# Optimization experiments

Measured on AMD Instinct MI355X. Metric: run time of the kernel, lower is better.

Reference implementation:

```python
import jax, jax.numpy as jnp
import numpy as np

B = 16384
D = 384
K = 256
BETAS = (0.05, 0.25, 0.6)  # per-level commitment costs


def setup_inputs() -> dict:
    key = jax.random.key(0)
    k0, k1, k2, kc0, kc1, kc2 = jax.random.split(key, 6)
    return {
        "l0": jax.random.normal(k0, (B, 4, D), dtype=jnp.float32),
        "l1": jax.random.normal(k1, (B, 16, D), dtype=jnp.float32),
        "l2": jax.random.normal(k2, (B, 16, D), dtype=jnp.float32),
        "cb0": jax.random.normal(kc0, (K, D), dtype=jnp.float32),
        "cb1": jax.random.normal(kc1, (K, D), dtype=jnp.float32),
        "cb2": jax.random.normal(kc2, (K, D), dtype=jnp.float32),
    }


def _vq(x, cb, beta):
    # x: (B, T, D), cb: (K, D) -> d2: (B, T, K)
    d2 = (jnp.sum(x * x, axis=-1, keepdims=True)
          - 2.0 * jnp.einsum('btd,kd->btk', x, cb)
          + jnp.sum(cb * cb, axis=-1))
    idx = jnp.argmin(d2, axis=-1)            # (B, T) nearest codebook entry
    q = cb[idx]                              # (B, T, D) gather
    # EMA-VQ: codebook updated by EMA, loss is commitment term only
    loss = beta * jnp.mean((jax.lax.stop_gradient(q) - x) ** 2)
    q_st = x + jax.lax.stop_gradient(q - x)  # straight-through estimator
    return q_st, loss, idx


def reference(l0, l1, l2, cb0, cb1, cb2):
    q0, loss0, idx0 = _vq(l0, cb0, BETAS[0])
    q1, loss1, idx1 = _vq(l1, cb1, BETAS[1])
    q2, loss2, idx2 = _vq(l2, cb2, BETAS[2])
    total_vq_loss = loss0 + loss1 + loss2
    return (q0, q1, q2, total_vq_loss, idx0, idx1, idx2)
```

## Files before the change

kernel.cpp:

```cpp
#include <hip/hip_runtime.h>

static constexpr int KN  = 256;
static constexpr int DD  = 384;
static constexpr int DD4 = 96;
static constexpr int TM  = 64;
#define FLAG_MARGIN 0.005f

typedef __attribute__((ext_vector_type(8)))  short bf16x8;
typedef __attribute__((ext_vector_type(16))) float f32x16;
typedef __attribute__((ext_vector_type(4)))  short short4v;

__device__ __forceinline__ unsigned short f2bf_rne(float x) {
  unsigned u = __float_as_uint(x);
  return (unsigned short)((u + 0x7fffu + ((u >> 16) & 1u)) >> 16);
}

__device__ __forceinline__ void g2lds16(const void* g, void* l) {
  __builtin_amdgcn_global_load_lds(
      (const __attribute__((address_space(1))) unsigned int*)g,
      (__attribute__((address_space(3))) unsigned int*)l, 16, 0, 0);
}

__device__ __forceinline__ float emu_sq_pairwise384(const float* __restrict__ p) {
  float S[4];
#pragma unroll
  for (int blk = 0; blk < 4; ++blk) {
    const float* b = p + blk * 96;
    float r[8];
#pragma unroll
    for (int l = 0; l < 8; ++l) r[l] = __fmul_rn(b[l], b[l]);
    for (int j = 8; j < 96; j += 8) {
#pragma unroll
      for (int l = 0; l < 8; ++l) r[l] = __fadd_rn(r[l], __fmul_rn(b[j + l], b[j + l]));
    }
    float t1 = __fadd_rn(__fadd_rn(r[0], r[1]), __fadd_rn(r[2], r[3]));
    float t2 = __fadd_rn(__fadd_rn(r[4], r[5]), __fadd_rn(r[6], r[7]));
    S[blk] = __fadd_rn(t1, t2);
  }
  return __fadd_rn(__fadd_rn(S[0], S[1]), __fadd_rn(S[2], S[3]));
}

__device__ __forceinline__ float emu_dot384_np(const float* __restrict__ x,
                                               const float* __restrict__ c) {
  float s[16];
#pragma unroll
  for (int t = 0; t < 16; ++t) s[t] = 0.f;
  for (int j = 0; j < 384; j += 16) {
#pragma unroll
    for (int t = 0; t < 16; ++t)
      s[t] = __fadd_rn(__fmul_rn(x[j + t], c[j + t]), s[t]);
  }
  float w0 = __fadd_rn(__fadd_rn(s[0], s[4]), __fadd_rn(s[8],  s[12]));
  float w1 = __fadd_rn(__fadd_rn(s[1], s[5]), __fadd_rn(s[9],  s[13]));
  float w2 = __fadd_rn(__fadd_rn(s[2], s[6]), __fadd_rn(s[10], s[14]));
  float w3 = __fadd_rn(__fadd_rn(s[3], s[7]), __fadd_rn(s[11], s[15]));
  return __fadd_rn(__fadd_rn(w0, w1), __fadd_rn(w2, w3));
}

__global__ __launch_bounds__(256) void prep_kernel(const float* __restrict__ c0,
                                                   const float* __restrict__ c1,
                                                   const float* __restrict__ c2,
                                                   float* __restrict__ e2,
                                                   double* __restrict__ delta,
                                                   short* __restrict__ fragbase) {
  int bid = blockIdx.x;
  if (bid < 3) {
    const float* cb = (bid == 0) ? c0 : ((bid == 1) ? c1 : c2);
    e2[bid * KN + threadIdx.x] = emu_sq_pairwise384(cb + (size_t)threadIdx.x * DD);
    if (threadIdx.x == 0) delta[bid] = 0.0;
    return;
  }
  int sb = bid - 3;
  int lvl = sb / 48;
  int blk48 = sb - lvl * 48;
  const float* cb = (lvl == 0) ? c0 : ((lvl == 1) ? c1 : c2);
  short* frag = fragbase + (size_t)lvl * 196608;
  int gid = blk48 * 256 + threadIdx.x;
  int e = gid / 48;
  int g = gid - e * 48;
  const float4* s4 = reinterpret_cast<const float4*>(cb) + (size_t)e * 96 + g * 2;
  float4 v0 = s4[0], v1 = s4[1];
  float xs[8] = {v0.x, v0.y, v0.z, v0.w, v1.x, v1.y, v1.z, v1.w};
  short h[8], l[8];
#pragma unroll
  for (int i = 0; i < 8; ++i) {
    h[i] = (short)f2bf_rne(xs[i]);
    float hf = __uint_as_float((unsigned)(unsigned short)h[i] << 16);
    l[i] = (short)f2bf_rne(xs[i] - hf);
  }
  int c = g >> 2, rem = g & 3, ks = rem >> 1, hs = rem & 1;
  int t = e >> 5, lane = (e & 31) + (hs << 5);
  size_t blk = (((size_t)(c * 8 + t) * 2 + ks) * 2);
  short* dh = frag + blk * 512 + lane * 8;
  short* dl = dh + 512;
  *reinterpret_cast<bf16x8*>(dh) = *reinterpret_cast<const bf16x8*>(h);
  *reinterpret_cast<bf16x8*>(dl) = *reinterpret_cast<const bf16x8*>(l);
}

__global__ __launch_bounds__(256) void vq_main(
    const float* __restrict__ X0, const float* __restrict__ X1, const float* __restrict__ X2,
    const float* __restrict__ C0, const float* __restrict__ C1, const float* __restrict__ C2,
    const short* __restrict__ FRAGBASE,
    const float* __restrict__ E2A,
    float* __restrict__ QBASE,
    float* __restrict__ IDXBASE,
    unsigned char* __restrict__ FLAGBASE,
    double* __restrict__ PART,
    int nb0, int nb1)
{
  __shared__ __align__(16) short cb_lds[16384];
  __shared__ __align__(16) short x_lds[4224];
  __shared__ int idx_s[TM];
  __shared__ float xx_s[TM];
  __shared__ float cand_b1[2][TM];
  __shared__ int   cand_i1[2][TM];
  __shared__ float cand_b2[2][TM];

  const int bid = blockIdx.x;
  int lvl, lb;
  if (bid < nb0)            { lvl = 0; lb = bid; }
  else if (bid < nb0 + nb1) { lvl = 1; lb = bid - nb0; }
  else                      { lvl = 2; lb = bid - nb0 - nb1; }
  const float* X  = (lvl == 0) ? X0 : ((lvl == 1) ? X1 : X2);
  const float* CBF32 = (lvl == 0) ? C0 : ((lvl == 1) ? C1 : C2);
  const short* CBFRAG = FRAGBASE + (size_t)lvl * 196608;
  const float* E2 = E2A + lvl * KN;
  const size_t rowbase = (lvl == 0) ? 0 : ((lvl == 1) ? (size_t)nb0 * TM
                                                      : (size_t)(nb0 + nb1) * TM);
  float* Q = QBASE + rowbase * DD;
  float* IDXO = IDXBASE + rowbase;
  unsigned char* FLAG = FLAGBASE + rowbase;
  const size_t row0 = (size_t)lb * TM;

  const float4* X4 = reinterpret_cast<const float4*>(X);

  f32x16 acc[4];
  {
    f32x16 z;
#pragma unroll
    for (int i = 0; i < 16; ++i) z[i] = 0.f;
#pragma unroll
    for (int ct = 0; ct < 4; ++ct) acc[ct] = z;
  }
  const int tid  = threadIdx.x;
  const int wid  = tid >> 6, lane = tid & 63;
  const int lr   = lane & 31, hi = lane >> 5;
  const int wr   = wid >> 1, wc = wid & 1;
  float xx0 = 0.f, xx1 = 0.f;

#pragma unroll 1
  for (int c = 0; c < 12; ++c) {
    {
      const char* gsrc = (const char*)CBFRAG + (size_t)c * 32768 + tid * 16;
#pragma unroll
      for (int s = 0; s < 8; ++s)
        g2lds16(gsrc + s * 4096, (char*)cb_lds + tid * 16 + s * 4096);
    }
#pragma unroll
    for (int i = 0; i < 2; ++i) {
      int idx = tid + i * 256;
      int r = idx >> 3, k4 = idx & 7;
      float4 v = X4[(row0 + (size_t)r) * DD4 + c * 8 + k4];
      float pp = v.x * v.x + v.y * v.y + v.z * v.z + v.w * v.w;
      if (i == 0) xx0 += pp; else xx1 += pp;
      float xs[4] = {v.x, v.y, v.z, v.w};
      short h[4], l[4];
#pragma unroll
      for (int e = 0; e < 4; ++e) {
        h[e] = (short)f2bf_rne(xs[e]);
        float hf = __uint_as_float((unsigned)(unsigned short)h[e] << 16);
        l[e] = (short)f2bf_rne(xs[e] - hf);
      }
      int rt = r >> 5, ks = k4 >> 2, hs = (k4 >> 1) & 1;
      int off_h = ((rt * 2 + ks) * 2) * 528 + hs * 264 + (r & 31) * 8 + (k4 & 1) * 4;
      *reinterpret_cast<short4v*>(&x_lds[off_h])       = *reinterpret_cast<short4v*>(h);
      *reinterpret_cast<short4v*>(&x_lds[off_h + 528]) = *reinterpret_cast<short4v*>(l);
    }
    __syncthreads();

#pragma unroll 1
    for (int ks = 0; ks < 2; ++ks) {
      const int abase = ((wr * 2 + ks) * 2) * 528 + hi * 264 + lr * 8;
      bf16x8 ah = *reinterpret_cast<const bf16x8*>(&x_lds[abase]);
      bf16x8 al = *reinterpret_cast<const bf16x8*>(&x_lds[abase + 528]);
      const bf16x8* bb = reinterpret_cast<const bf16x8*>(cb_lds);
#pragma unroll
      for (int ct = 0; ct < 4; ++ct) {
        int t = wc * 4 + ct;
        bf16x8 bh = bb[((t * 2 + ks) * 2 + 0) * 64 + lane];
        bf16x8 bl = bb[((t * 2 + ks) * 2 + 1) * 64 + lane];
        acc[ct] = __builtin_amdgcn_mfma_f32_32x32x16_bf16(ah, bh, acc[ct], 0, 0, 0);
        acc[ct] = __builtin_amdgcn_mfma_f32_32x32x16_bf16(ah, bl, acc[ct], 0, 0, 0);
        acc[ct] = __builtin_amdgcn_mfma_f32_32x32x16_bf16(al, bh, acc[ct], 0, 0, 0);
      }
    }
    __syncthreads();
  }

#pragma unroll
  for (int m = 1; m < 8; m <<= 1) {
    xx0 += __shfl_xor(xx0, m);
    xx1 += __shfl_xor(xx1, m);
  }
  if ((lane & 7) == 0) {
    xx_s[tid >> 3]        = xx0;
    xx_s[(tid >> 3) + 32] = xx1;
  }

  float e2v[4];
#pragma unroll
  for (int ct = 0; ct < 4; ++ct) e2v[ct] = E2[wc * 128 + ct * 32 + lr];

#pragma unroll
  for (int v = 0; v < 16; ++v) {
    int rloc = (v & 3) + 8 * (v >> 2) + 4 * hi;
    int row = wr * 32 + rloc;
    float b1 = 1e30f; int i1 = 0x7fffffff;
#pragma unroll
    for (int ct = 0; ct < 4; ++ct) {
      float sc = e2v[ct] - 2.0f * acc[ct][v];
      int col = wc * 128 + ct * 32 + lr;
      if (sc < b1) { b1 = sc; i1 = col; }
    }
#pragma unroll
    for (int m = 1; m < 32; m <<= 1) {
      float ob = __shfl_xor(b1, m);
      int   oi = __shfl_xor(i1, m);
      if (ob < b1 || (ob == b1 && oi < i1)) { b1 = ob; i1 = oi; }
    }
    float b2 = 1e30f;
#pragma unroll
    for (int ct = 0; ct < 4; ++ct) {
      float sc = e2v[ct] - 2.0f * acc[ct][v];
      int col = wc * 128 + ct * 32 + lr;
      if (col != i1 && sc < b2) b2 = sc;
    }
#pragma unroll
    for (int m = 1; m < 32; m <<= 1) {
      float ob = __shfl_xor(b2, m);
      if (ob < b2) b2 = ob;
    }
    if (lr == 0) {
      cand_b1[wc][row] = b1; cand_i1[wc][row] = i1; cand_b2[wc][row] = b2;
    }
  }
  __syncthreads();

  double lrow = 0.0;
  if (tid < TM) {
    float a1 = cand_b1[0][tid], a2 = cand_b2[0][tid];
    int   ai = cand_i1[0][tid];
    float c1 = cand_b1[1][tid], c2 = cand_b2[1][tid];
    int   ci = cand_i1[1][tid];
    float b1; int i1; float b2;
    if (c1 < a1 || (c1 == a1 && ci < ai)) {
      b1 = c1; i1 = ci; b2 = (a1 < c2) ? a1 : c2;
    } else {
      b1 = a1; i1 = ai; b2 = (c1 < a2) ? c1 : a2;
    }
    idx_s[tid] = i1;
    IDXO[row0 + tid] = (float)i1;
    FLAG[row0 + tid] = (b2 - b1 < FLAG_MARGIN) ? 1 : 0;
    lrow = (double)xx_s[tid] + (double)b1;
  }
  if (tid < 64) {
#pragma unroll
    for (int m = 1; m < 64; m <<= 1) lrow += __shfl_xor(lrow, m);
    if (tid == 0) PART[bid] = lrow;
  }
  __syncthreads();

  const float4* CB4 = reinterpret_cast<const float4*>(CBF32);
  float4* Q4 = reinterpret_cast<float4*>(Q);
  for (int i = tid; i < TM * DD4; i += 256) {
    int r = i / DD4;
    int cc = i - r * DD4;
    Q4[(row0 + (size_t)r) * DD4 + cc] = CB4[(size_t)idx_s[r] * DD4 + cc];
  }
}

__global__ __launch_bounds__(256) void vq_refine(
    const float* __restrict__ X0, const float* __restrict__ X1, const float* __restrict__ X2,
    const float* __restrict__ C0, const float* __restrict__ C1, const float* __restrict__ C2,
    const float* __restrict__ E2A,
    const unsigned char* __restrict__ F0, const unsigned char* __restrict__ F1,
    const unsigned char* __restrict__ F2,
    int r0, int r1, int r2,
    float* __restrict__ Q0, float* __restrict__ Q1, float* __restrict__ Q2,
    float* __restrict__ I0, float* __restrict__ I1, float* __restrict__ I2,
    double* __restrict__ DELTA)
{
  const int lane   = threadIdx.x & 63;
  const int gwave  = (blockIdx.x * blockDim.x + threadIdx.x) >> 6;
  const int nwaves = (gridDim.x * blockDim.x) >> 6;
  const int ntot = r0 + r1 + r2;

  for (int base = gwave * 64; base < ntot; base += nwaves * 64) {
    int lvl, lb;
    const float *X, *CB; const unsigned char* FLAG; float *Q, *IDXO;
    if (base < r0)           { lvl = 0; lb = base;            X = X0; CB = C0; FLAG = F0; Q = Q0; IDXO = I0; }
    else if (base < r0 + r1) { lvl = 1; lb = base - r0;       X = X1; CB = C1; FLAG = F1; Q = Q1; IDXO = I1; }
    else                     { lvl = 2; lb = base - r0 - r1;  X = X2; CB = C2; FLAG = F2; Q = Q2; IDXO = I2; }
    const float* E2EMU = E2A + lvl * KN;

    unsigned char f = FLAG[lb + lane];
    unsigned long long mask = __ballot(f != 0);
    while (mask) {
      int bit = __ffsll((long long)mask) - 1;
      mask &= mask - 1;
      const int r = lb + bit;
      const float* xr = X + (size_t)r * DD;
      const float xx = emu_sq_pairwise384(xr);

      float best = 1e30f; int bidx = 0x7fffffff;
#pragma unroll
      for (int t = 0; t < 4; ++t) {
        int k = lane * 4 + t;
        const float* ck = CB + (size_t)k * DD;
        float E = emu_dot384_np(xr, ck);
        float s = __fadd_rn(__fsub_rn(xx, __fmul_rn(2.0f, E)), E2EMU[k]);
        if (s < best || (s == best && k < bidx)) { best = s; bidx = k; }
      }
#pragma unroll
      for (int m = 1; m < 64; m <<= 1) {
        float ob = __shfl_xor(best, m);
        int   oi = __shfl_xor(bidx, m);
        if (ob < best || (ob == best && oi < bidx)) { best = ob; bidx = oi; }
      }

      const int old = (int)IDXO[r];
      if (bidx != old) {
        const float* cn = CB + (size_t)bidx * DD;
        const float* co = CB + (size_t)old * DD;
        double dl = 0.0;
        for (int d = lane; d < DD; d += 64) {
          float xv = xr[d];
          float qn = cn[d], qo = co[d];
          Q[(size_t)r * DD + d] = qn;
          double en = (double)qn - (double)xv;
          double eo = (double)qo - (double)xv;
          dl += en * en - eo * eo;
        }
#pragma unroll
        for (int m = 1; m < 64; m <<= 1) dl += __shfl_xor(dl, m);
        if (lane == 0) {
          atomicAdd(DELTA + lvl, dl);
          IDXO[r] = (float)bidx;
        }
      }
    }
  }
}

__global__ void finalize_kernel(const double* __restrict__ p0, int n0, double w0,
                                const double* __restrict__ p1, int n1, double w1,
                                const double* __restrict__ p2, int n2, double w2,
                                const double* __restrict__ delta,
                                float* __restrict__ out) {
  __shared__ double red[4];
  int tid = threadIdx.x;
  double s0 = 0.0, s1 = 0.0, s2 = 0.0;
  for (int i = tid; i < n0; i += 256) s0 += p0[i];
  for (int i = tid; i < n1; i += 256) s1 += p1[i];
  for (int i = tid; i < n2; i += 256) s2 += p2[i];
  double v = s0 * w0 + s1 * w1 + s2 * w2;
#pragma unroll
  for (int m = 1; m < 64; m <<= 1) v += __shfl_xor(v, m);
  if ((tid & 63) == 0) red[tid >> 6] = v;
  __syncthreads();
  if (tid == 0)
    out[0] = (float)(red[0] + red[1] + red[2] + red[3]
                     + delta[0] * w0 + delta[1] * w1 + delta[2] * w2);
}

extern "C" void kernel_launch(void* const* d_in, const int* in_sizes, int n_in,
                              void* d_out, int out_size, void* d_ws, size_t ws_size,
                              hipStream_t stream) {
  const float* l0  = (const float*)d_in[0];
  const float* l1  = (const float*)d_in[1];
  const float* l2  = (const float*)d_in[2];
  const float* cb0 = (const float*)d_in[3];
  const float* cb1 = (const float*)d_in[4];
  const float* cb2 = (const float*)d_in[5];

  const size_t n_q0 = (size_t)in_sizes[0];
  const size_t n_q1 = (size_t)in_sizes[1];
  const size_t n_q2 = (size_t)in_sizes[2];
  const int r0 = (int)(n_q0 / DD);
  const int r1 = (int)(n_q1 / DD);
  const int r2 = (int)(n_q2 / DD);

  float* out   = (float*)d_out;
  float* q0    = out;
  float* q1    = q0 + n_q0;
  float* q2    = q1 + n_q1;
  float* lossp = q2 + n_q2;
  float* idx0  = lossp + 1;
  float* idx1  = idx0 + r0;
  float* idx2  = idx1 + r1;

  float*  e2    = (float*)d_ws;
  double* part  = (double*)((char*)d_ws + 4096);
  double* delta = (double*)((char*)d_ws + 4096 + 73728);
  unsigned char* flag0 = (unsigned char*)d_ws + 4096 + 73728 + 1024;
  unsigned char* flag1 = flag0 + r0;
  unsigned char* flag2 = flag1 + r1;
  short* cbf0 = (short*)((char*)d_ws + (1 << 20));

  const int nb0 = r0 / TM, nb1 = r1 / TM, nb2 = r2 / TM;
  double* p0 = part;
  double* p1 = p0 + nb0;
  double* p2 = p1 + nb1;

  prep_kernel<<<147, 256, 0, stream>>>(cb0, cb1, cb2, e2, delta, cbf0);

  vq_main<<<nb0 + nb1 + nb2, 256, 0, stream>>>(
      l0, l1, l2, cb0, cb1, cb2, cbf0, e2,
      q0, idx0, flag0, part, nb0, nb1);

  vq_refine<<<512, 256, 0, stream>>>(l0, l1, l2, cb0, cb1, cb2, e2,
                                     flag0, flag1, flag2, r0, r1, r2,
                                     q0, q1, q2, idx0, idx1, idx2, delta);

  const double w0 = 0.05 / ((double)r0 * DD);
  const double w1 = 0.25 / ((double)r1 * DD);
  const double w2 = 0.60 / ((double)r2 * DD);
  finalize_kernel<<<1, 256, 0, stream>>>(p0, nb0, w0, p1, nb1, w1, p2, nb2, w2,
                                         delta, lossp);
}
```

Measured before the change: 770.7 us.

## Double-buffer codebook tiles and load X fragments straight into registers

Codebook chunks are now double-buffered in LDS and prefetched one chunk ahead, with a single barrier per iteration instead of two. The X rows are read from global memory directly into per-lane MFMA operand registers (register prefetch of the next chunk), which removes the x_lds staging buffer and its writes. The norm reduction becomes a single cross-half shuffle. In exchange each tile of X is loaded twice (once per column wave) and LDS use doubles for the codebook, which may reduce occupancy.

```diff
diff --git a/kernel.cpp b/kernel.cpp
--- a/kernel.cpp
+++ b/kernel.cpp
@@ -8,7 +8,6 @@
 
 typedef __attribute__((ext_vector_type(8)))  short bf16x8;
 typedef __attribute__((ext_vector_type(16))) float f32x16;
-typedef __attribute__((ext_vector_type(4)))  short short4v;
 
 __device__ __forceinline__ unsigned short f2bf_rne(float x) {
   unsigned u = __float_as_uint(x);
@@ -19,6 +18,19 @@
   __builtin_amdgcn_global_load_lds(
       (const __attribute__((address_space(1))) unsigned int*)g,
       (__attribute__((address_space(3))) unsigned int*)l, 16, 0, 0);
+}
+
+__device__ __forceinline__ void cvt8(float4 a, float4 b, bf16x8& h, bf16x8& l,
+                                     float& xx) {
+  float v[8] = {a.x, a.y, a.z, a.w, b.x, b.y, b.z, b.w};
+#pragma unroll
+  for (int i = 0; i < 8; ++i) {
+    xx += v[i] * v[i];
+    unsigned short hh = f2bf_rne(v[i]);
+    float hf = __uint_as_float((unsigned)hh << 16);
+    h[i] = (short)hh;
+    l[i] = (short)f2bf_rne(v[i] - hf);
+  }
 }
 
 __device__ __forceinline__ float emu_sq_pairwise384(const float* __restrict__ p) {
@@ -108,8 +120,7 @@
     double* __restrict__ PART,
     int nb0, int nb1)
 {
-  __shared__ __align__(16) short cb_lds[16384];
-  __shared__ __align__(16) short x_lds[4224];
+  __shared__ __align__(16) short cb_lds[2][16384];
   __shared__ int idx_s[TM];
   __shared__ float xx_s[TM];
   __shared__ float cand_b1[2][TM];
@@ -132,80 +143,69 @@
   unsigned char* FLAG = FLAGBASE + rowbase;
   const size_t row0 = (size_t)lb * TM;
 
-  const float4* X4 = reinterpret_cast<const float4*>(X);
-
-  f32x16 acc[4];
-  {
-    f32x16 z;
-#pragma unroll
-    for (int i = 0; i < 16; ++i) z[i] = 0.f;
-#pragma unroll
-    for (int ct = 0; ct < 4; ++ct) acc[ct] = z;
-  }
   const int tid  = threadIdx.x;
   const int wid  = tid >> 6, lane = tid & 63;
   const int lr   = lane & 31, hi = lane >> 5;
   const int wr   = wid >> 1, wc = wid & 1;
-  float xx0 = 0.f, xx1 = 0.f;
+
+  const float4* X4 = reinterpret_cast<const float4*>(X);
+  const float4* xrow = X4 + (row0 + (size_t)(wr * 32 + lr)) * DD4 + hi * 2;
+
+  f32x16 acc[4];
+  {
+    f32x16 z;
+#pragma unroll
+    for (int i = 0; i < 16; ++i) z[i] = 0.f;
+#pragma unroll
+    for (int ct = 0; ct < 4; ++ct) acc[ct] = z;
+  }
+  float xx = 0.f;
+
+  float4 xr0 = xrow[0], xr1 = xrow[1], xr2 = xrow[4], xr3 = xrow[5];
+  {
+    const char* gsrc = (const char*)CBFRAG + (size_t)tid * 16;
+#pragma unroll
+    for (int s = 0; s < 8; ++s)
+      g2lds16(gsrc + s * 4096, (char*)cb_lds[0] + tid * 16 + s * 4096);
+  }
+  __syncthreads();
 
 #pragma unroll 1
   for (int c = 0; c < 12; ++c) {
-    {
-      const char* gsrc = (const char*)CBFRAG + (size_t)c * 32768 + tid * 16;
+    bf16x8 ah0, al0, ah1, al1;
+    cvt8(xr0, xr1, ah0, al0, xx);
+    cvt8(xr2, xr3, ah1, al1, xx);
+
+    if (c < 11) {
+      const float4* xp = xrow + (c + 1) * 8;
+      xr0 = xp[0]; xr1 = xp[1]; xr2 = xp[4]; xr3 = xp[5];
+      const char* gsrc = (const char*)CBFRAG + (size_t)(c + 1) * 32768 + tid * 16;
+      char* dst = (char*)cb_lds[(c + 1) & 1] + tid * 16;
 #pragma unroll
       for (int s = 0; s < 8; ++s)
-        g2lds16(gsrc + s * 4096, (char*)cb_lds + tid * 16 + s * 4096);
-    }
-#pragma unroll
-    for (int i = 0; i < 2; ++i) {
-      int idx = tid + i * 256;
-      int r = idx >> 3, k4 = idx & 7;
-      float4 v = X4[(row0 + (size_t)r) * DD4 + c * 8 + k4];
-      float pp = v.x * v.x + v.y * v.y + v.z * v.z + v.w * v.w;
-      if (i == 0) xx0 += pp; else xx1 += pp;
-      float xs[4] = {v.x, v.y, v.z, v.w};
-      short h[4], l[4];
-#pragma unroll
-      for (int e = 0; e < 4; ++e) {
-        h[e] = (short)f2bf_rne(xs[e]);
-        float hf = __uint_as_float((unsigned)(unsigned short)h[e] << 16);
-        l[e] = (short)f2bf_rne(xs[e] - hf);
-      }
-      int rt = r >> 5, ks = k4 >> 2, hs = (k4 >> 1) & 1;
-      int off_h = ((rt * 2 + ks) * 2) * 528 + hs * 264 + (r & 31) * 8 + (k4 & 1) * 4;
-      *reinterpret_cast<short4v*>(&x_lds[off_h])       = *reinterpret_cast<short4v*>(h);
-      *reinterpret_cast<short4v*>(&x_lds[off_h + 528]) = *reinterpret_cast<short4v*>(l);
-    }
-    __syncthreads();
-
-#pragma unroll 1
-    for (int ks = 0; ks < 2; ++ks) {
-      const int abase = ((wr * 2 + ks) * 2) * 528 + hi * 264 + lr * 8;
-      bf16x8 ah = *reinterpret_cast<const bf16x8*>(&x_lds[abase]);
-      bf16x8 al = *reinterpret_cast<const bf16x8*>(&x_lds[abase + 528]);
-      const bf16x8* bb = reinterpret_cast<const bf16x8*>(cb_lds);
-#pragma unroll
-      for (int ct = 0; ct < 4; ++ct) {
-        int t = wc * 4 + ct;
-        bf16x8 bh = bb[((t * 2 + ks) * 2 + 0) * 64 + lane];
-        bf16x8 bl = bb[((t * 2 + ks) * 2 + 1) * 64 + lane];
-        acc[ct] = __builtin_amdgcn_mfma_f32_32x32x16_bf16(ah, bh, acc[ct], 0, 0, 0);
-        acc[ct] = __builtin_amdgcn_mfma_f32_32x32x16_bf16(ah, bl, acc[ct], 0, 0, 0);
-        acc[ct] = __builtin_amdgcn_mfma_f32_32x32x16_bf16(al, bh, acc[ct], 0, 0, 0);
-      }
-    }
-    __syncthreads();
-  }
-
-#pragma unroll
-  for (int m = 1; m < 8; m <<= 1) {
-    xx0 += __shfl_xor(xx0, m);
-    xx1 += __shfl_xor(xx1, m);
-  }
-  if ((lane & 7) == 0) {
-    xx_s[tid >> 3]        = xx0;
-    xx_s[(tid >> 3) + 32] = xx1;
-  }
+        g2lds16(gsrc + s * 4096, dst + s * 4096);
+    }
+
+    const bf16x8* bb = reinterpret_cast<const bf16x8*>(cb_lds[c & 1]);
+#pragma unroll
+    for (int ct = 0; ct < 4; ++ct) {
+      int t = wc * 4 + ct;
+      bf16x8 bh0 = bb[((t * 2 + 0) * 2 + 0) * 64 + lane];
+      bf16x8 bl0 = bb[((t * 2 + 0) * 2 + 1) * 64 + lane];
+      bf16x8 bh1 = bb[((t * 2 + 1) * 2 + 0) * 64 + lane];
+      bf16x8 bl1 = bb[((t * 2 + 1) * 2 + 1) * 64 + lane];
+      acc[ct] = __builtin_amdgcn_mfma_f32_32x32x16_bf16(ah0, bh0, acc[ct], 0, 0, 0);
+      acc[ct] = __builtin_amdgcn_mfma_f32_32x32x16_bf16(ah0, bl0, acc[ct], 0, 0, 0);
+      acc[ct] = __builtin_amdgcn_mfma_f32_32x32x16_bf16(al0, bh0, acc[ct], 0, 0, 0);
+      acc[ct] = __builtin_amdgcn_mfma_f32_32x32x16_bf16(ah1, bh1, acc[ct], 0, 0, 0);
+      acc[ct] = __builtin_amdgcn_mfma_f32_32x32x16_bf16(ah1, bl1, acc[ct], 0, 0, 0);
+      acc[ct] = __builtin_amdgcn_mfma_f32_32x32x16_bf16(al1, bh1, acc[ct], 0, 0, 0);
+    }
+    if (c != 11) __syncthreads();
+  }
+
+  xx += __shfl_xor(xx, 32);
+  if (wc == 0 && hi == 0) xx_s[wr * 32 + lr] = xx;
 
   float e2v[4];
 #pragma unroll
```

Measured after the change: 1.005 ms. +30.4%, slower.
